# Kernel optimization log

Hardware: AMD Instinct MI355X
Metric: run time of the kernel (lower is better)

Reference implementation:

```python
import jax, jax.numpy as jnp
import numpy as np

B, I, D = 4, 8192, 1024
R_MIN, R_MAX = 0.4, 0.99


def setup_inputs() -> dict:
    key = jax.random.key(0)
    k_x, k_u = jax.random.split(key)
    x = jax.random.normal(k_x, (B, I, D), dtype=jnp.float32)
    # nu_logs initialized as in LRU.__init__: ring-uniform radii in [r_min, r_max]
    u = jax.random.uniform(k_u, (D,), dtype=jnp.float32)
    nus = -jnp.log(u * (R_MAX**2 - R_MIN**2) + R_MIN**2) / 2.0
    nu_logs = jnp.log(nus)
    return {"x": x, "nu_logs": nu_logs}


def reference(x, nu_logs):
    # lambdas in (0,1): per-channel decay; gammas normalize input magnitude
    lambdas = jnp.exp(-jnp.exp(nu_logs))            # [d]
    gammas = jnp.sqrt(1.0 - jnp.abs(lambdas) ** 2)  # [d]
    values = gammas[None, None, :] * x              # [b, i, d]
    a = jnp.broadcast_to(lambdas[None, None, :], values.shape)  # [b, i, d]

    # inclusive discounted cumsum (left-to-right): h_t = lambda * h_{t-1} + v_t
    def combine(c1, c2):
        a1, b1 = c1
        a2, b2 = c2
        return (a1 * a2, a2 * b1 + b2)

    _, hidden = jax.lax.associative_scan(combine, (a, values), axis=1)
    return hidden  # [b, i, d]
```

## Files before the change

kernel.cpp:

```cpp
#include <hip/hip_runtime.h>
#include <math.h>


#define B_  4
#define I_  8192
#define D_  1024
#define C_  256
#define L_  32
#define D4  (D_ / 4)

__device__ __forceinline__ void load_lam_gam(const float* __restrict__ nu_logs,
                                             int d4, float4& lam, float4& gam) {
    const float* nl = nu_logs + d4 * 4;
    lam.x = expf(-expf(nl[0]));
    lam.y = expf(-expf(nl[1]));
    lam.z = expf(-expf(nl[2]));
    lam.w = expf(-expf(nl[3]));
    gam.x = sqrtf(1.0f - lam.x * lam.x);
    gam.y = sqrtf(1.0f - lam.y * lam.y);
    gam.z = sqrtf(1.0f - lam.z * lam.z);
    gam.w = sqrtf(1.0f - lam.w * lam.w);
}

__global__ __launch_bounds__(256) void lru_phase1(const float4* __restrict__ x,
                                                  const float* __restrict__ nu_logs,
                                                  float4* __restrict__ carry) {
    int tid = blockIdx.x * 256 + threadIdx.x;
    int d4 = tid & (D4 - 1);
    int c  = (tid >> 8) & (C_ - 1);
    int b  = tid >> 16;

    float4 lam, gam;
    load_lam_gam(nu_logs, d4, lam, gam);

    int idx = (b * I_ + c * L_) * D4 + d4;
    float4 h = {0.f, 0.f, 0.f, 0.f};
#pragma unroll 8
    for (int t = 0; t < L_; ++t) {
        float4 v = x[idx];
        h.x = fmaf(lam.x, h.x, gam.x * v.x);
        h.y = fmaf(lam.y, h.y, gam.y * v.y);
        h.z = fmaf(lam.z, h.z, gam.z * v.z);
        h.w = fmaf(lam.w, h.w, gam.w * v.w);
        idx += D4;
    }
    carry[(b * C_ + c) * D4 + d4] = h;
}

__global__ __launch_bounds__(C_) void lru_phase2(const float* __restrict__ nu_logs,
                                                 float4* __restrict__ carry) {
    __shared__ float4 buf[C_];
    int c  = threadIdx.x;
    int d4 = blockIdx.x & (D4 - 1);
    int b  = blockIdx.x >> 8;

    const float* nl = nu_logs + d4 * 4;
    float4 p;
    p.x = expf(-expf(nl[0]) * (float)L_);
    p.y = expf(-expf(nl[1]) * (float)L_);
    p.z = expf(-expf(nl[2]) * (float)L_);
    p.w = expf(-expf(nl[3]) * (float)L_);

    int gidx = (b * C_ + c) * D4 + d4;
    float4 val = carry[gidx];
    buf[c] = val;

    for (int off = 1; off < C_; off <<= 1) {
        __syncthreads();
        float4 prev = (c >= off) ? buf[c - off] : make_float4(0.f, 0.f, 0.f, 0.f);
        __syncthreads();
        if (c >= off) {
            val.x = fmaf(p.x, prev.x, val.x);
            val.y = fmaf(p.y, prev.y, val.y);
            val.z = fmaf(p.z, prev.z, val.z);
            val.w = fmaf(p.w, prev.w, val.w);
            buf[c] = val;
        }
        p.x *= p.x; p.y *= p.y; p.z *= p.z; p.w *= p.w;
    }
    __syncthreads();
    float4 excl = (c == 0) ? make_float4(0.f, 0.f, 0.f, 0.f) : buf[c - 1];
    carry[gidx] = excl;
}

__global__ __launch_bounds__(256) void lru_phase3(const float4* __restrict__ x,
                                                  const float* __restrict__ nu_logs,
                                                  const float4* __restrict__ carry,
                                                  float4* __restrict__ out) {
    int tid = blockIdx.x * 256 + threadIdx.x;
    int d4 = tid & (D4 - 1);
    int c  = (tid >> 8) & (C_ - 1);
    int b  = tid >> 16;

    float4 lam, gam;
    load_lam_gam(nu_logs, d4, lam, gam);

    float4 h = carry[(b * C_ + c) * D4 + d4];
    int idx = (b * I_ + c * L_) * D4 + d4;
#pragma unroll 8
    for (int t = 0; t < L_; ++t) {
        float4 v = x[idx];
        h.x = fmaf(lam.x, h.x, gam.x * v.x);
        h.y = fmaf(lam.y, h.y, gam.y * v.y);
        h.z = fmaf(lam.z, h.z, gam.z * v.z);
        h.w = fmaf(lam.w, h.w, gam.w * v.w);
        out[idx] = h;
        idx += D4;
    }
}

extern "C" void kernel_launch(void* const* d_in, const int* in_sizes, int n_in,
                              void* d_out, int out_size, void* d_ws, size_t ws_size,
                              hipStream_t stream) {
    const float4* x       = (const float4*)d_in[0];
    const float*  nu_logs = (const float*)d_in[1];
    float4*       out     = (float4*)d_out;
    float4*       carry   = (float4*)d_ws;

    dim3 blk(256);
    dim3 grd_big((B_ * C_ * D4) / 256);
    dim3 grd_p2(B_ * D4);

    lru_phase1<<<grd_big, blk, 0, stream>>>(x, nu_logs, carry);
    lru_phase2<<<grd_p2, dim3(C_), 0, stream>>>(nu_logs, carry);
    lru_phase3<<<grd_big, blk, 0, stream>>>(x, nu_logs, carry, out);
}
```

Before: 267.4 us.

## Fuse three scan phases into one cooperative kernel with grid syncs

Replaces the three separate kernel launches (chunk reduce, carry scan, chunk rescan) with a single cooperative kernel of 1024 blocks that uses grid.sync between phases. Output stores become nontemporal. The aim is to remove launch gaps and inter-kernel overhead, and to keep x resident for the second pass. The cost is two grid-wide barriers, and the launch requires all 1024 blocks to be co-resident (4 per CU via launch bounds).

```diff
diff --git a/kernel.cpp b/kernel.cpp
--- a/kernel.cpp
+++ b/kernel.cpp
@@ -1,5 +1,8 @@
 #include <hip/hip_runtime.h>
+#include <hip/hip_cooperative_groups.h>
 #include <math.h>
+
+namespace cg = cooperative_groups;
 
 
 #define B_  4
@@ -9,9 +12,23 @@
 #define L_  32
 #define D4  (D_ / 4)
 
-__device__ __forceinline__ void load_lam_gam(const float* __restrict__ nu_logs,
-                                             int d4, float4& lam, float4& gam) {
+typedef float f32x4 __attribute__((ext_vector_type(4)));
+
+__global__ __launch_bounds__(256, 4) void lru_fused(
+        const float4* __restrict__ x,
+        const float* __restrict__ nu_logs,
+        float4* __restrict__ carry,
+        float4* __restrict__ out) {
+    cg::grid_group grid = cg::this_grid();
+    __shared__ float4 buf[C_];
+
+    const int blk = blockIdx.x;
+    const int d4  = threadIdx.x;
+    const int c   = blk & (C_ - 1);
+    const int b   = blk >> 8;
+
     const float* nl = nu_logs + d4 * 4;
+    float4 lam, gam;
     lam.x = expf(-expf(nl[0]));
     lam.y = expf(-expf(nl[1]));
     lam.z = expf(-expf(nl[2]));
@@ -20,108 +37,87 @@
     gam.y = sqrtf(1.0f - lam.y * lam.y);
     gam.z = sqrtf(1.0f - lam.z * lam.z);
     gam.w = sqrtf(1.0f - lam.w * lam.w);
-}
 
-__global__ __launch_bounds__(256) void lru_phase1(const float4* __restrict__ x,
-                                                  const float* __restrict__ nu_logs,
-                                                  float4* __restrict__ carry) {
-    int tid = blockIdx.x * 256 + threadIdx.x;
-    int d4 = tid & (D4 - 1);
-    int c  = (tid >> 8) & (C_ - 1);
-    int b  = tid >> 16;
+    {
+        float4 h = {0.f, 0.f, 0.f, 0.f};
+        int idx = (b * I_ + c * L_) * D4 + d4;
+#pragma unroll 8
+        for (int t = 0; t < L_; ++t) {
+            float4 v = x[idx];
+            h.x = fmaf(lam.x, h.x, gam.x * v.x);
+            h.y = fmaf(lam.y, h.y, gam.y * v.y);
+            h.z = fmaf(lam.z, h.z, gam.z * v.z);
+            h.w = fmaf(lam.w, h.w, gam.w * v.w);
+            idx += D4;
+        }
+        carry[(b * C_ + c) * D4 + d4] = h;
+    }
 
-    float4 lam, gam;
-    load_lam_gam(nu_logs, d4, lam, gam);
+    grid.sync();
 
-    int idx = (b * I_ + c * L_) * D4 + d4;
-    float4 h = {0.f, 0.f, 0.f, 0.f};
+    {
+        const int c2 = threadIdx.x;
+        const int dd = blk & (D4 - 1);
+        const int b2 = blk >> 8;
+
+        const float* nl2 = nu_logs + dd * 4;
+        float4 p;
+        p.x = expf(-expf(nl2[0]) * (float)L_);
+        p.y = expf(-expf(nl2[1]) * (float)L_);
+        p.z = expf(-expf(nl2[2]) * (float)L_);
+        p.w = expf(-expf(nl2[3]) * (float)L_);
+
+        const int gidx = (b2 * C_ + c2) * D4 + dd;
+        float4 val = carry[gidx];
+        buf[c2] = val;
+
+        for (int off = 1; off < C_; off <<= 1) {
+            __syncthreads();
+            float4 prev = (c2 >= off) ? buf[c2 - off]
+                                      : make_float4(0.f, 0.f, 0.f, 0.f);
+            __syncthreads();
+            if (c2 >= off) {
+                val.x = fmaf(p.x, prev.x, val.x);
+                val.y = fmaf(p.y, prev.y, val.y);
+                val.z = fmaf(p.z, prev.z, val.z);
+                val.w = fmaf(p.w, prev.w, val.w);
+                buf[c2] = val;
+            }
+            p.x *= p.x; p.y *= p.y; p.z *= p.z; p.w *= p.w;
+        }
+        __syncthreads();
+        float4 excl = (c2 == 0) ? make_float4(0.f, 0.f, 0.f, 0.f) : buf[c2 - 1];
+        carry[gidx] = excl;
+    }
+
+    grid.sync();
+
+    {
+        float4 h = carry[(b * C_ + c) * D4 + d4];
+        int idx = (b * I_ + c * L_) * D4 + d4;
 #pragma unroll 8
-    for (int t = 0; t < L_; ++t) {
-        float4 v = x[idx];
-        h.x = fmaf(lam.x, h.x, gam.x * v.x);
-        h.y = fmaf(lam.y, h.y, gam.y * v.y);
-        h.z = fmaf(lam.z, h.z, gam.z * v.z);
-        h.w = fmaf(lam.w, h.w, gam.w * v.w);
-        idx += D4;
-    }
-    carry[(b * C_ + c) * D4 + d4] = h;
-}
-
-__global__ __launch_bounds__(C_) void lru_phase2(const float* __restrict__ nu_logs,
-                                                 float4* __restrict__ carry) {
-    __shared__ float4 buf[C_];
-    int c  = threadIdx.x;
-    int d4 = blockIdx.x & (D4 - 1);
-    int b  = blockIdx.x >> 8;
-
-    const float* nl = nu_logs + d4 * 4;
-    float4 p;
-    p.x = expf(-expf(nl[0]) * (float)L_);
-    p.y = expf(-expf(nl[1]) * (float)L_);
-    p.z = expf(-expf(nl[2]) * (float)L_);
-    p.w = expf(-expf(nl[3]) * (float)L_);
-
-    int gidx = (b * C_ + c) * D4 + d4;
-    float4 val = carry[gidx];
-    buf[c] = val;
-
-    for (int off = 1; off < C_; off <<= 1) {
-        __syncthreads();
-        float4 prev = (c >= off) ? buf[c - off] : make_float4(0.f, 0.f, 0.f, 0.f);
-        __syncthreads();
-        if (c >= off) {
-            val.x = fmaf(p.x, prev.x, val.x);
-            val.y = fmaf(p.y, prev.y, val.y);
-            val.z = fmaf(p.z, prev.z, val.z);
-            val.w = fmaf(p.w, prev.w, val.w);
-            buf[c] = val;
+        for (int t = 0; t < L_; ++t) {
+            float4 v = x[idx];
+            h.x = fmaf(lam.x, h.x, gam.x * v.x);
+            h.y = fmaf(lam.y, h.y, gam.y * v.y);
+            h.z = fmaf(lam.z, h.z, gam.z * v.z);
+            h.w = fmaf(lam.w, h.w, gam.w * v.w);
+            __builtin_nontemporal_store(*(const f32x4*)&h, (f32x4*)&out[idx]);
+            idx += D4;
         }
-        p.x *= p.x; p.y *= p.y; p.z *= p.z; p.w *= p.w;
-    }
-    __syncthreads();
-    float4 excl = (c == 0) ? make_float4(0.f, 0.f, 0.f, 0.f) : buf[c - 1];
-    carry[gidx] = excl;
-}
-
-__global__ __launch_bounds__(256) void lru_phase3(const float4* __restrict__ x,
-                                                  const float* __restrict__ nu_logs,
-                                                  const float4* __restrict__ carry,
-                                                  float4* __restrict__ out) {
-    int tid = blockIdx.x * 256 + threadIdx.x;
-    int d4 = tid & (D4 - 1);
-    int c  = (tid >> 8) & (C_ - 1);
-    int b  = tid >> 16;
-
-    float4 lam, gam;
-    load_lam_gam(nu_logs, d4, lam, gam);
-
-    float4 h = carry[(b * C_ + c) * D4 + d4];
-    int idx = (b * I_ + c * L_) * D4 + d4;
-#pragma unroll 8
-    for (int t = 0; t < L_; ++t) {
-        float4 v = x[idx];
-        h.x = fmaf(lam.x, h.x, gam.x * v.x);
-        h.y = fmaf(lam.y, h.y, gam.y * v.y);
-        h.z = fmaf(lam.z, h.z, gam.z * v.z);
-        h.w = fmaf(lam.w, h.w, gam.w * v.w);
-        out[idx] = h;
-        idx += D4;
     }
 }
 
 extern "C" void kernel_launch(void* const* d_in, const int* in_sizes, int n_in,
                               void* d_out, int out_size, void* d_ws, size_t ws_size,
                               hipStream_t stream) {
+    (void)in_sizes; (void)n_in; (void)out_size; (void)ws_size;
     const float4* x       = (const float4*)d_in[0];
     const float*  nu_logs = (const float*)d_in[1];
     float4*       out     = (float4*)d_out;
     float4*       carry   = (float4*)d_ws;
 
-    dim3 blk(256);
-    dim3 grd_big((B_ * C_ * D4) / 256);
-    dim3 grd_p2(B_ * D4);
-
-    lru_phase1<<<grd_big, blk, 0, stream>>>(x, nu_logs, carry);
-    lru_phase2<<<grd_p2, dim3(C_), 0, stream>>>(nu_logs, carry);
-    lru_phase3<<<grd_big, blk, 0, stream>>>(x, nu_logs, carry, out);
+    void* args[] = {(void*)&x, (void*)&nu_logs, (void*)&carry, (void*)&out};
+    hipLaunchCooperativeKernel((void*)lru_fused, dim3(B_ * C_), dim3(256),
+                               args, 0, stream);
 }
```

Result: slower. 503.3 us (+88.2%).

## Replace carry scan kernel with per-chunk serial prefix recomputation in output pass

Applied to the files above, without the earlier changes.

Removes the separate shared-memory scan kernel; each output thread instead folds all preceding chunk carries with the chunk decay power to get its starting state. Loads in the per-chunk loops are also batched eight at a time to raise memory-level parallelism. This saves a kernel launch and a carry write-back. In exchange it adds quadratic carry reads from cache and long serial dependency chains for later chunks, which unbalances the threads.

```diff
diff --git a/kernel.cpp b/kernel.cpp
--- a/kernel.cpp
+++ b/kernel.cpp
@@ -22,9 +22,17 @@
     gam.w = sqrtf(1.0f - lam.w * lam.w);
 }
 
-__global__ __launch_bounds__(256) void lru_phase1(const float4* __restrict__ x,
-                                                  const float* __restrict__ nu_logs,
-                                                  float4* __restrict__ carry) {
+__device__ __forceinline__ void step(float4& h, const float4 lam,
+                                     const float4 gam, const float4 v) {
+    h.x = fmaf(lam.x, h.x, gam.x * v.x);
+    h.y = fmaf(lam.y, h.y, gam.y * v.y);
+    h.z = fmaf(lam.z, h.z, gam.z * v.z);
+    h.w = fmaf(lam.w, h.w, gam.w * v.w);
+}
+
+__global__ __launch_bounds__(256) void lru_carry(const float4* __restrict__ x,
+                                                 const float* __restrict__ nu_logs,
+                                                 float4* __restrict__ carry) {
     int tid = blockIdx.x * 256 + threadIdx.x;
     int d4 = tid & (D4 - 1);
     int c  = (tid >> 8) & (C_ - 1);
@@ -35,58 +43,33 @@
 
     int idx = (b * I_ + c * L_) * D4 + d4;
     float4 h = {0.f, 0.f, 0.f, 0.f};
-#pragma unroll 8
-    for (int t = 0; t < L_; ++t) {
-        float4 v = x[idx];
-        h.x = fmaf(lam.x, h.x, gam.x * v.x);
-        h.y = fmaf(lam.y, h.y, gam.y * v.y);
-        h.z = fmaf(lam.z, h.z, gam.z * v.z);
-        h.w = fmaf(lam.w, h.w, gam.w * v.w);
-        idx += D4;
+#pragma unroll
+    for (int tt = 0; tt < L_; tt += 8) {
+        float4 v0 = x[idx + 0 * D4];
+        float4 v1 = x[idx + 1 * D4];
+        float4 v2 = x[idx + 2 * D4];
+        float4 v3 = x[idx + 3 * D4];
+        float4 v4 = x[idx + 4 * D4];
+        float4 v5 = x[idx + 5 * D4];
+        float4 v6 = x[idx + 6 * D4];
+        float4 v7 = x[idx + 7 * D4];
+        step(h, lam, gam, v0);
+        step(h, lam, gam, v1);
+        step(h, lam, gam, v2);
+        step(h, lam, gam, v3);
+        step(h, lam, gam, v4);
+        step(h, lam, gam, v5);
+        step(h, lam, gam, v6);
+        step(h, lam, gam, v7);
+        idx += 8 * D4;
     }
     carry[(b * C_ + c) * D4 + d4] = h;
 }
 
-__global__ __launch_bounds__(C_) void lru_phase2(const float* __restrict__ nu_logs,
-                                                 float4* __restrict__ carry) {
-    __shared__ float4 buf[C_];
-    int c  = threadIdx.x;
-    int d4 = blockIdx.x & (D4 - 1);
-    int b  = blockIdx.x >> 8;
-
-    const float* nl = nu_logs + d4 * 4;
-    float4 p;
-    p.x = expf(-expf(nl[0]) * (float)L_);
-    p.y = expf(-expf(nl[1]) * (float)L_);
-    p.z = expf(-expf(nl[2]) * (float)L_);
-    p.w = expf(-expf(nl[3]) * (float)L_);
-
-    int gidx = (b * C_ + c) * D4 + d4;
-    float4 val = carry[gidx];
-    buf[c] = val;
-
-    for (int off = 1; off < C_; off <<= 1) {
-        __syncthreads();
-        float4 prev = (c >= off) ? buf[c - off] : make_float4(0.f, 0.f, 0.f, 0.f);
-        __syncthreads();
-        if (c >= off) {
-            val.x = fmaf(p.x, prev.x, val.x);
-            val.y = fmaf(p.y, prev.y, val.y);
-            val.z = fmaf(p.z, prev.z, val.z);
-            val.w = fmaf(p.w, prev.w, val.w);
-            buf[c] = val;
-        }
-        p.x *= p.x; p.y *= p.y; p.z *= p.z; p.w *= p.w;
-    }
-    __syncthreads();
-    float4 excl = (c == 0) ? make_float4(0.f, 0.f, 0.f, 0.f) : buf[c - 1];
-    carry[gidx] = excl;
-}
-
-__global__ __launch_bounds__(256) void lru_phase3(const float4* __restrict__ x,
-                                                  const float* __restrict__ nu_logs,
-                                                  const float4* __restrict__ carry,
-                                                  float4* __restrict__ out) {
+__global__ __launch_bounds__(256) void lru_scan_out(const float4* __restrict__ x,
+                                                    const float* __restrict__ nu_logs,
+                                                    const float4* __restrict__ carry,
+                                                    float4* __restrict__ out) {
     int tid = blockIdx.x * 256 + threadIdx.x;
     int d4 = tid & (D4 - 1);
     int c  = (tid >> 8) & (C_ - 1);
@@ -95,33 +78,59 @@
     float4 lam, gam;
     load_lam_gam(nu_logs, d4, lam, gam);
 
-    float4 h = carry[(b * C_ + c) * D4 + d4];
+    const float* nl = nu_logs + d4 * 4;
+    float4 pL;
+    pL.x = expf(-expf(nl[0]) * (float)L_);
+    pL.y = expf(-expf(nl[1]) * (float)L_);
+    pL.z = expf(-expf(nl[2]) * (float)L_);
+    pL.w = expf(-expf(nl[3]) * (float)L_);
+
+    float4 h = {0.f, 0.f, 0.f, 0.f};
+    const float4* cb = carry + b * C_ * D4 + d4;
+#pragma unroll 4
+    for (int j = 0; j < c; ++j) {
+        float4 cj = cb[j * D4];
+        h.x = fmaf(pL.x, h.x, cj.x);
+        h.y = fmaf(pL.y, h.y, cj.y);
+        h.z = fmaf(pL.z, h.z, cj.z);
+        h.w = fmaf(pL.w, h.w, cj.w);
+    }
+
     int idx = (b * I_ + c * L_) * D4 + d4;
-#pragma unroll 8
-    for (int t = 0; t < L_; ++t) {
-        float4 v = x[idx];
-        h.x = fmaf(lam.x, h.x, gam.x * v.x);
-        h.y = fmaf(lam.y, h.y, gam.y * v.y);
-        h.z = fmaf(lam.z, h.z, gam.z * v.z);
-        h.w = fmaf(lam.w, h.w, gam.w * v.w);
-        out[idx] = h;
-        idx += D4;
+#pragma unroll
+    for (int tt = 0; tt < L_; tt += 8) {
+        float4 v0 = x[idx + 0 * D4];
+        float4 v1 = x[idx + 1 * D4];
+        float4 v2 = x[idx + 2 * D4];
+        float4 v3 = x[idx + 3 * D4];
+        float4 v4 = x[idx + 4 * D4];
+        float4 v5 = x[idx + 5 * D4];
+        float4 v6 = x[idx + 6 * D4];
+        float4 v7 = x[idx + 7 * D4];
+        step(h, lam, gam, v0); out[idx + 0 * D4] = h;
+        step(h, lam, gam, v1); out[idx + 1 * D4] = h;
+        step(h, lam, gam, v2); out[idx + 2 * D4] = h;
+        step(h, lam, gam, v3); out[idx + 3 * D4] = h;
+        step(h, lam, gam, v4); out[idx + 4 * D4] = h;
+        step(h, lam, gam, v5); out[idx + 5 * D4] = h;
+        step(h, lam, gam, v6); out[idx + 6 * D4] = h;
+        step(h, lam, gam, v7); out[idx + 7 * D4] = h;
+        idx += 8 * D4;
     }
 }
 
 extern "C" void kernel_launch(void* const* d_in, const int* in_sizes, int n_in,
                               void* d_out, int out_size, void* d_ws, size_t ws_size,
                               hipStream_t stream) {
+    (void)in_sizes; (void)n_in; (void)out_size; (void)ws_size;
     const float4* x       = (const float4*)d_in[0];
     const float*  nu_logs = (const float*)d_in[1];
     float4*       out     = (float4*)d_out;
     float4*       carry   = (float4*)d_ws;
 
     dim3 blk(256);
-    dim3 grd_big((B_ * C_ * D4) / 256);
-    dim3 grd_p2(B_ * D4);
+    dim3 grd((B_ * C_ * D4) / 256);
 
-    lru_phase1<<<grd_big, blk, 0, stream>>>(x, nu_logs, carry);
-    lru_phase2<<<grd_p2, dim3(C_), 0, stream>>>(nu_logs, carry);
-    lru_phase3<<<grd_big, blk, 0, stream>>>(x, nu_logs, carry, out);
+    lru_carry<<<grd, blk, 0, stream>>>(x, nu_logs, carry);
+    lru_scan_out<<<grd, blk, 0, stream>>>(x, nu_logs, carry, out);
 }
```

Result: no change. 266.8 us (-0.2%).
